# Kernel tuning notes

Hardware: AMD Instinct MI355X
Metric: run time of the kernel (lower is better)

## Reference

```python
import jax, jax.numpy as jnp
import numpy as np

B, E, NH = 32, 4096, 32
D = E // NH            # head_dim = 128
MAX_TOKENS = 2048
MAX_POS = 1536         # next_pos values in [0, MAX_POS); max pinned so max_k is static


def setup_inputs() -> dict:
    key = jax.random.key(0)
    k0, k1, k2, k3, k4, k5 = jax.random.split(key, 6)
    x = jax.random.normal(k0, (B, 1, E), jnp.float32)
    next_pos = jax.random.randint(k1, (B,), 0, MAX_POS, jnp.int32)
    next_pos = next_pos.at[0].set(MAX_POS - 1)  # pin max so sliced cache length is fixed
    scale = 0.02
    Wq = jax.random.normal(k2, (D, E), jnp.float32) * scale
    Wk = jax.random.normal(k3, (D, E), jnp.float32) * scale
    Wv = jax.random.normal(k4, (D, E), jnp.float32) * scale
    kv_cache = jax.random.normal(k5, (2, B, MAX_TOKENS, D), jnp.float32) * scale
    return {"x": x, "Wq": Wq, "Wk": Wk, "Wv": Wv, "kv_cache": kv_cache, "next_pos": next_pos}


def reference(x, Wq, Wk, Wv, kv_cache, next_pos):
    # x: (B, 1, E); torch Linear(y = x @ W.T)
    q = jnp.einsum('bse,de->bsd', x, Wq)  # (B,1,D)
    k = jnp.einsum('bse,de->bsd', x, Wk)
    v = jnp.einsum('bse,de->bsd', x, Wv)

    # scatter the new step into the cache at each sequence's next_pos
    bidx = jnp.arange(x.shape[0])
    kv = kv_cache.at[0, bidx, next_pos].set(k[:, 0])
    kv = kv.at[1, bidx, next_pos].set(v[:, 0])

    next_pos_new = next_pos + 1
    max_k = int(jax.device_get(jnp.max(next_pos_new)))  # static given pinned next_pos

    k_cache = kv[0, :, :max_k]  # (B, max_k, D)
    v_cache = kv[1, :, :max_k]

    scores = jnp.einsum('bsd,btd->bst', q, k_cache) * (D ** -0.5)  # (B,1,max_k)
    # Faithful to torch: (max_k,max_k) tril mask broadcasts scores to (B,max_k,max_k)
    tril = jnp.tril(jnp.ones((max_k, max_k), dtype=bool))
    masked = jnp.where(tril[None], scores, -jnp.inf)  # (B, max_k, max_k)
    attn = jax.nn.softmax(masked, axis=-1)
    out = attn @ v_cache  # (B, max_k, D)
    return out
```

## Files before the change

kernel.cpp:

```cpp
#include <hip/hip_runtime.h>
#include <math.h>

#define CHUNK 32

__global__ void proj_kernel(const float* __restrict__ x,
                            const float* __restrict__ Wq,
                            const float* __restrict__ Wk,
                            const float* __restrict__ Wv,
                            float* __restrict__ qkv,
                            int B, int E, int D)
{
    int d = blockIdx.x;
    int b = blockIdx.y;
    int lane = threadIdx.x;
    const float* xrow = x + (size_t)b * E;
    size_t woff = (size_t)d * E;
    float aq = 0.f, ak = 0.f, av = 0.f;
    for (int i = lane * 4; i < E; i += 64 * 4) {
        float4 x4 = *(const float4*)(xrow + i);
        float4 q4 = *(const float4*)(Wq + woff + i);
        float4 k4 = *(const float4*)(Wk + woff + i);
        float4 v4 = *(const float4*)(Wv + woff + i);
        aq += x4.x*q4.x + x4.y*q4.y + x4.z*q4.z + x4.w*q4.w;
        ak += x4.x*k4.x + x4.y*k4.y + x4.z*k4.z + x4.w*k4.w;
        av += x4.x*v4.x + x4.y*v4.y + x4.z*v4.z + x4.w*v4.w;
    }
    #pragma unroll
    for (int off = 32; off >= 1; off >>= 1) {
        aq += __shfl_xor(aq, off, 64);
        ak += __shfl_xor(ak, off, 64);
        av += __shfl_xor(av, off, 64);
    }
    if (lane == 0) {
        qkv[(size_t)b * D + d] = aq;
        qkv[((size_t)B + b) * D + d] = ak;
        qkv[((size_t)2 * B + b) * D + d] = av;
    }
}

__global__ void score_chunk_kernel(const float* __restrict__ kv,
                                   const float* __restrict__ qkv,
                                   const int* __restrict__ next_pos,
                                   float* __restrict__ s_out,
                                   float* __restrict__ m_out,
                                   float* __restrict__ l_out,
                                   float* __restrict__ acc_out,
                                   int B, int D, int T, int MT, int NC, float scale)
{
    int c = blockIdx.x;
    int b = blockIdx.y;
    int tid = threadIdx.x;
    int wave = tid >> 6;
    int lane = tid & 63;
    int l16 = lane & 15;
    int g16 = lane >> 4;

    __shared__ float s_sh[CHUNK];
    __shared__ float w_sh[CHUNK];
    __shared__ float part[2][128];

    int np = next_pos[b];
    int t0 = c * CHUNK;
    const float* q    = qkv + (size_t)b * D;
    const float* knew = qkv + ((size_t)B + b) * D;
    const float* vnew = qkv + ((size_t)2 * B + b) * D;
    const float* kbase = kv + (size_t)b * MT * D;
    const float* vbase = kv + ((size_t)B + b) * MT * D;

    float4 qa = *(const float4*)(q + l16 * 8);
    float4 qb = *(const float4*)(q + l16 * 8 + 4);

    #pragma unroll
    for (int p = 0; p < 2; ++p) {
        int j = wave * 8 + p * 4 + g16;
        int t = t0 + j;
        const float* krow = (t == np) ? knew : (kbase + (size_t)t * D);
        float4 ka = *(const float4*)(krow + l16 * 8);
        float4 kb = *(const float4*)(krow + l16 * 8 + 4);
        float ps = qa.x*ka.x + qa.y*ka.y + qa.z*ka.z + qa.w*ka.w
                 + qb.x*kb.x + qb.y*kb.y + qb.z*kb.z + qb.w*kb.w;
        ps += __shfl_xor(ps, 1, 64);
        ps += __shfl_xor(ps, 2, 64);
        ps += __shfl_xor(ps, 4, 64);
        ps += __shfl_xor(ps, 8, 64);
        if (l16 == 0) {
            float sv = (t < T) ? ps * scale : -1e30f;
            s_sh[j] = sv;
            if (t < T) s_out[(size_t)b * T + t] = sv;
        }
    }
    __syncthreads();

    if (wave == 0) {
        float sv = s_sh[lane & 31];
        float m = sv;
        #pragma unroll
        for (int off = 16; off >= 1; off >>= 1)
            m = fmaxf(m, __shfl_xor(m, off, 64));
        float w = __expf(sv - m);
        w_sh[lane & 31] = w;
        float l = w;
        #pragma unroll
        for (int off = 16; off >= 1; off >>= 1)
            l += __shfl_xor(l, off, 64);
        if (lane == 0) {
            m_out[(size_t)b * NC + c] = m;
            l_out[(size_t)b * NC + c] = l;
        }
    }
    __syncthreads();

    int gg = tid >> 7;
    int d = tid & 127;
    float a = 0.f;
    #pragma unroll
    for (int jj = 0; jj < 16; ++jj) {
        int j = gg * 16 + jj;
        int t = t0 + j;
        const float* vrow = (t == np) ? vnew : (vbase + (size_t)t * D);
        a += w_sh[j] * vrow[d];
    }
    part[gg][d] = a;
    __syncthreads();
    if (tid < 128)
        acc_out[((size_t)b * NC + c) * D + tid] = part[0][tid] + part[1][tid];
}

__global__ void out_kernel(const float* __restrict__ kv,
                           const float* __restrict__ qkv,
                           const int* __restrict__ next_pos,
                           const float* __restrict__ s_in,
                           const float* __restrict__ m_in,
                           const float* __restrict__ l_in,
                           const float* __restrict__ acc_in,
                           float* __restrict__ out,
                           int B, int D, int T, int MT, int NC)
{
    int c = blockIdx.x;
    int b = blockIdx.y;
    int tid = threadIdx.x;

    __shared__ float vs[CHUNK * 128];
    __shared__ float w_sh[CHUNK];
    __shared__ float rl_sh[CHUNK];
    __shared__ float M_sh;

    int np = next_pos[b];
    int t0 = c * CHUNK;
    const float* mrow = m_in + (size_t)b * NC;
    const float* lrow = l_in + (size_t)b * NC;

    if (tid < 64) {
        float mv = (tid <= c) ? mrow[tid] : -1e30f;
        #pragma unroll
        for (int off = 32; off >= 1; off >>= 1)
            mv = fmaxf(mv, __shfl_xor(mv, off, 64));
        if (tid == 0) M_sh = mv;
    }
    __syncthreads();
    float M = M_sh;

    const float* vbase = kv + ((size_t)B + b) * MT * D;
    const float4* vnew4 = (const float4*)(qkv + ((size_t)2 * B + b) * D);
    const float4* vbase4 = (const float4*)vbase;

    float A = 0.f;
    if (tid < 128) {
        const float* arow0 = acc_in + (size_t)b * NC * D;
        for (int cc = 0; cc < c; ++cc) {
            float e = __expf(mrow[cc] - M);
            A += e * arow0[(size_t)cc * D + tid];
        }
    } else {
        int t2 = tid - 128;
        #pragma unroll
        for (int r = 0; r < 8; ++r) {
            int i4 = t2 + r * 128;
            int j = i4 >> 5;
            int t = t0 + j;
            float4 vv = (t == np) ? vnew4[i4 & 31]
                                  : vbase4[(size_t)t * 32 + (i4 & 31)];
            ((float4*)vs)[i4] = vv;
        }
        if (t2 < CHUNK) {
            int t = t0 + t2;
            w_sh[t2] = (t < T) ? __expf(s_in[(size_t)b * T + t] - M) : 0.f;
        }
    }
    __syncthreads();

    if (tid < CHUNK) {
        float L = 0.f;
        for (int cc = 0; cc < c; ++cc)
            L += lrow[cc] * __expf(mrow[cc] - M);
        for (int r = 0; r <= tid; ++r)
            L += w_sh[r];
        rl_sh[tid] = 1.0f / L;
    }
    __syncthreads();

    if (tid < 128) {
        float* orow = out + ((size_t)b * T + t0) * (size_t)D + tid;
        #pragma unroll
        for (int j = 0; j < CHUNK; ++j) {
            int t = t0 + j;
            if (t >= T) break;
            A += w_sh[j] * vs[j * 128 + tid];
            orow[(size_t)j * D] = A * rl_sh[j];
        }
    }
}

extern "C" void kernel_launch(void* const* d_in, const int* in_sizes, int n_in,
                              void* d_out, int out_size, void* d_ws, size_t ws_size,
                              hipStream_t stream) {
    const float* x        = (const float*)d_in[0];
    const float* Wq       = (const float*)d_in[1];
    const float* Wk       = (const float*)d_in[2];
    const float* Wv       = (const float*)d_in[3];
    const float* kv       = (const float*)d_in[4];
    const int*   next_pos = (const int*)d_in[5];
    float* out = (float*)d_out;

    const int B  = in_sizes[5];
    const int E  = in_sizes[0] / B;
    const int D  = in_sizes[1] / E;
    const int T  = out_size / (B * D);
    const int MT = in_sizes[4] / (2 * B * D);
    const int NC = (T + CHUNK - 1) / CHUNK;

    float* ws   = (float*)d_ws;
    float* qkv  = ws;
    float* s    = qkv + (size_t)3 * B * D;
    float* m    = s + (size_t)B * T;
    float* l    = m + (size_t)B * NC;
    float* acc  = l + (size_t)B * NC;

    const float scale = 1.0f / sqrtf((float)D);

    proj_kernel<<<dim3(D, B), 64, 0, stream>>>(x, Wq, Wk, Wv, qkv, B, E, D);
    score_chunk_kernel<<<dim3(NC, B), 256, 0, stream>>>(kv, qkv, next_pos,
                                                        s, m, l, acc,
                                                        B, D, T, MT, NC, scale);
    out_kernel<<<dim3(NC, B), 256, 0, stream>>>(kv, qkv, next_pos,
                                                s, m, l, acc, out,
                                                B, D, T, MT, NC);
}
```

Baseline: 138.4 us.

## Add per-batch prefix scan kernel to replace quadratic carry recomputation in out_kernel

Adds a scan kernel that computes the running max, carry denominator and carry accumulator per chunk once per batch, so each out_kernel block reads its carry directly instead of looping over all previous chunks. The old approach cost work quadratic in the number of chunks. The score kernel's V accumulation is also changed to use float4 loads across 8 row groups. The cost is one extra kernel launch, a serial loop over 48 chunks in only 32 blocks, and extra workspace.

```diff
diff --git a/kernel.cpp b/kernel.cpp
--- a/kernel.cpp
+++ b/kernel.cpp
@@ -2,6 +2,7 @@
 #include <math.h>
 
 #define CHUNK 32
+#define MAXNC 128
 
 __global__ void proj_kernel(const float* __restrict__ x,
                             const float* __restrict__ Wq,
@@ -57,15 +58,15 @@
 
     __shared__ float s_sh[CHUNK];
     __shared__ float w_sh[CHUNK];
-    __shared__ float part[2][128];
+    __shared__ float part[8][128];
 
     int np = next_pos[b];
     int t0 = c * CHUNK;
     const float* q    = qkv + (size_t)b * D;
     const float* knew = qkv + ((size_t)B + b) * D;
-    const float* vnew = qkv + ((size_t)2 * B + b) * D;
     const float* kbase = kv + (size_t)b * MT * D;
-    const float* vbase = kv + ((size_t)B + b) * MT * D;
+    const float4* vnew4 = (const float4*)(qkv + ((size_t)2 * B + b) * D);
+    const float4* vbase4 = (const float4*)(kv + ((size_t)B + b) * MT * D);
 
     float4 qa = *(const float4*)(q + l16 * 8);
     float4 qb = *(const float4*)(q + l16 * 8 + 4);
@@ -110,29 +111,79 @@
     }
     __syncthreads();
 
-    int gg = tid >> 7;
-    int d = tid & 127;
-    float a = 0.f;
+    int rg = tid >> 5;
+    int d4 = tid & 31;
+    float4 a4 = make_float4(0.f, 0.f, 0.f, 0.f);
     #pragma unroll
-    for (int jj = 0; jj < 16; ++jj) {
-        int j = gg * 16 + jj;
+    for (int p = 0; p < 4; ++p) {
+        int j = rg * 4 + p;
         int t = t0 + j;
-        const float* vrow = (t == np) ? vnew : (vbase + (size_t)t * D);
-        a += w_sh[j] * vrow[d];
-    }
-    part[gg][d] = a;
-    __syncthreads();
-    if (tid < 128)
-        acc_out[((size_t)b * NC + c) * D + tid] = part[0][tid] + part[1][tid];
+        float4 vv = (t == np) ? vnew4[d4] : vbase4[(size_t)t * 32 + d4];
+        float w = w_sh[j];
+        a4.x += w * vv.x; a4.y += w * vv.y; a4.z += w * vv.z; a4.w += w * vv.w;
+    }
+    ((float4*)&part[rg][d4 * 4])[0] = a4;
+    __syncthreads();
+    if (tid < 128) {
+        float s = 0.f;
+        #pragma unroll
+        for (int r = 0; r < 8; ++r) s += part[r][tid];
+        acc_out[((size_t)b * NC + c) * D + tid] = s;
+    }
+}
+
+__global__ void scan_kernel(const float* __restrict__ m_in,
+                            const float* __restrict__ l_in,
+                            const float* __restrict__ acc_in,
+                            float* __restrict__ Mc_out,
+                            float* __restrict__ carryL_out,
+                            float* __restrict__ carryA_out,
+                            int B, int D, int NC)
+{
+    int b = blockIdx.x;
+    int tid = threadIdx.x;
+
+    extern __shared__ float sh[];
+    float* accs = sh;
+    float* m_l  = sh + (size_t)NC * 128;
+    float* l_l  = m_l + NC;
+
+    const float4* asrc = (const float4*)(acc_in + (size_t)b * NC * D);
+    float4* adst = (float4*)accs;
+    for (int i = tid; i < NC * 32; i += 128)
+        adst[i] = asrc[i];
+    if (tid < NC) {
+        m_l[tid] = m_in[(size_t)b * NC + tid];
+        l_l[tid] = l_in[(size_t)b * NC + tid];
+    }
+    __syncthreads();
+
+    float M = -1e30f, A = 0.f, L = 0.f;
+    float* caout = carryA_out + (size_t)b * NC * D + tid;
+    for (int c = 0; c < NC; ++c) {
+        float mc = m_l[c];
+        float Mn = fmaxf(M, mc);
+        float e_old = __expf(M - Mn);
+        float Ac = A * e_old;
+        caout[(size_t)c * D] = Ac;
+        if (tid == 0) {
+            Mc_out[(size_t)b * NC + c] = Mn;
+            carryL_out[(size_t)b * NC + c] = L * e_old;
+        }
+        float e_c = __expf(mc - Mn);
+        A = Ac + e_c * accs[c * 128 + tid];
+        L = L * e_old + e_c * l_l[c];
+        M = Mn;
+    }
 }
 
 __global__ void out_kernel(const float* __restrict__ kv,
                            const float* __restrict__ qkv,
                            const int* __restrict__ next_pos,
                            const float* __restrict__ s_in,
-                           const float* __restrict__ m_in,
-                           const float* __restrict__ l_in,
-                           const float* __restrict__ acc_in,
+                           const float* __restrict__ Mc_in,
+                           const float* __restrict__ carryL_in,
+                           const float* __restrict__ carryA_in,
                            float* __restrict__ out,
                            int B, int D, int T, int MT, int NC)
 {
@@ -143,33 +194,20 @@
     __shared__ float vs[CHUNK * 128];
     __shared__ float w_sh[CHUNK];
     __shared__ float rl_sh[CHUNK];
-    __shared__ float M_sh;
 
     int np = next_pos[b];
     int t0 = c * CHUNK;
-    const float* mrow = m_in + (size_t)b * NC;
-    const float* lrow = l_in + (size_t)b * NC;
-
-    if (tid < 64) {
-        float mv = (tid <= c) ? mrow[tid] : -1e30f;
-        #pragma unroll
-        for (int off = 32; off >= 1; off >>= 1)
-            mv = fmaxf(mv, __shfl_xor(mv, off, 64));
-        if (tid == 0) M_sh = mv;
-    }
-    __syncthreads();
-    float M = M_sh;
-
-    const float* vbase = kv + ((size_t)B + b) * MT * D;
+    float M = Mc_in[(size_t)b * NC + c];
+
     const float4* vnew4 = (const float4*)(qkv + ((size_t)2 * B + b) * D);
-    const float4* vbase4 = (const float4*)vbase;
+    const float4* vbase4 = (const float4*)(kv + ((size_t)B + b) * MT * D);
 
     float A = 0.f;
     if (tid < 128) {
-        const float* arow0 = acc_in + (size_t)b * NC * D;
-        for (int cc = 0; cc < c; ++cc) {
-            float e = __expf(mrow[cc] - M);
-            A += e * arow0[(size_t)cc * D + tid];
+        A = carryA_in[((size_t)b * NC + c) * D + tid];
+        if (tid < CHUNK) {
+            int t = t0 + tid;
+            w_sh[tid] = (t < T) ? __expf(s_in[(size_t)b * T + t] - M) : 0.f;
         }
     } else {
         int t2 = tid - 128;
@@ -182,17 +220,11 @@
                                   : vbase4[(size_t)t * 32 + (i4 & 31)];
             ((float4*)vs)[i4] = vv;
         }
-        if (t2 < CHUNK) {
-            int t = t0 + t2;
-            w_sh[t2] = (t < T) ? __expf(s_in[(size_t)b * T + t] - M) : 0.f;
-        }
     }
     __syncthreads();
 
     if (tid < CHUNK) {
-        float L = 0.f;
-        for (int cc = 0; cc < c; ++cc)
-            L += lrow[cc] * __expf(mrow[cc] - M);
+        float L = carryL_in[(size_t)b * NC + c];
         for (int r = 0; r <= tid; ++r)
             L += w_sh[r];
         rl_sh[tid] = 1.0f / L;
@@ -229,12 +261,15 @@
     const int MT = in_sizes[4] / (2 * B * D);
     const int NC = (T + CHUNK - 1) / CHUNK;
 
-    float* ws   = (float*)d_ws;
-    float* qkv  = ws;
-    float* s    = qkv + (size_t)3 * B * D;
-    float* m    = s + (size_t)B * T;
-    float* l    = m + (size_t)B * NC;
-    float* acc  = l + (size_t)B * NC;
+    float* ws     = (float*)d_ws;
+    float* qkv    = ws;
+    float* s      = qkv + (size_t)3 * B * D;
+    float* m      = s + (size_t)B * T;
+    float* l      = m + (size_t)B * NC;
+    float* acc    = l + (size_t)B * NC;
+    float* Mc     = acc + (size_t)B * NC * D;
+    float* carryL = Mc + (size_t)B * NC;
+    float* carryA = carryL + (size_t)B * NC;
 
     const float scale = 1.0f / sqrtf((float)D);
 
@@ -242,7 +277,10 @@
     score_chunk_kernel<<<dim3(NC, B), 256, 0, stream>>>(kv, qkv, next_pos,
                                                         s, m, l, acc,
                                                         B, D, T, MT, NC, scale);
+    size_t scan_lds = ((size_t)NC * 128 + 2 * NC) * sizeof(float);
+    scan_kernel<<<dim3(B), 128, scan_lds, stream>>>(m, l, acc, Mc, carryL, carryA,
+                                                    B, D, NC);
     out_kernel<<<dim3(NC, B), 256, 0, stream>>>(kv, qkv, next_pos,
-                                                s, m, l, acc, out,
+                                                s, Mc, carryL, carryA, out,
                                                 B, D, T, MT, NC);
 }
```

Result: faster. 135.2 us (-2.3%).

## Fuse score and output kernels with flag-based chunk prefix sync

Applied to the files above, without the earlier changes.

Merges the score-chunk and output kernels into one kernel. Each chunk block publishes its unnormalized partial V accumulator and weight sum, then spin-waits on per-chunk flags for earlier chunks of the same batch row before doing the prefix combine. The max-subtraction in the softmax is dropped and raw exp(score) is used, which relies on scores being small. The projection kernel is reorganized so each block stages one row of each weight in shared memory and reuses it across all batch rows. The risks are overflow for large scores, and deadlock if dependent blocks are not co-resident; since blocks are ordered with lower chunks first, progress is likely.

```diff
diff --git a/kernel.cpp b/kernel.cpp
--- a/kernel.cpp
+++ b/kernel.cpp
@@ -2,200 +2,219 @@
 #include <math.h>
 
 #define CHUNK 32
+
+__device__ __forceinline__ float agent_load_f(const float* p) {
+    return __hip_atomic_load(p, __ATOMIC_RELAXED, __HIP_MEMORY_SCOPE_AGENT);
+}
+__device__ __forceinline__ void agent_store_f(float* p, float v) {
+    __hip_atomic_store(p, v, __ATOMIC_RELAXED, __HIP_MEMORY_SCOPE_AGENT);
+}
 
 __global__ void proj_kernel(const float* __restrict__ x,
                             const float* __restrict__ Wq,
                             const float* __restrict__ Wk,
                             const float* __restrict__ Wv,
                             float* __restrict__ qkv,
+                            int* __restrict__ flags, int nflags,
                             int B, int E, int D)
 {
     int d = blockIdx.x;
-    int b = blockIdx.y;
-    int lane = threadIdx.x;
-    const float* xrow = x + (size_t)b * E;
-    size_t woff = (size_t)d * E;
-    float aq = 0.f, ak = 0.f, av = 0.f;
-    for (int i = lane * 4; i < E; i += 64 * 4) {
-        float4 x4 = *(const float4*)(xrow + i);
-        float4 q4 = *(const float4*)(Wq + woff + i);
-        float4 k4 = *(const float4*)(Wk + woff + i);
-        float4 v4 = *(const float4*)(Wv + woff + i);
-        aq += x4.x*q4.x + x4.y*q4.y + x4.z*q4.z + x4.w*q4.w;
-        ak += x4.x*k4.x + x4.y*k4.y + x4.z*k4.z + x4.w*k4.w;
-        av += x4.x*v4.x + x4.y*v4.y + x4.z*v4.z + x4.w*v4.w;
-    }
-    #pragma unroll
-    for (int off = 32; off >= 1; off >>= 1) {
-        aq += __shfl_xor(aq, off, 64);
-        ak += __shfl_xor(ak, off, 64);
-        av += __shfl_xor(av, off, 64);
-    }
-    if (lane == 0) {
-        qkv[(size_t)b * D + d] = aq;
-        qkv[((size_t)B + b) * D + d] = ak;
-        qkv[((size_t)2 * B + b) * D + d] = av;
-    }
-}
-
-__global__ void score_chunk_kernel(const float* __restrict__ kv,
-                                   const float* __restrict__ qkv,
-                                   const int* __restrict__ next_pos,
-                                   float* __restrict__ s_out,
-                                   float* __restrict__ m_out,
-                                   float* __restrict__ l_out,
-                                   float* __restrict__ acc_out,
-                                   int B, int D, int T, int MT, int NC, float scale)
-{
-    int c = blockIdx.x;
-    int b = blockIdx.y;
     int tid = threadIdx.x;
     int wave = tid >> 6;
     int lane = tid & 63;
-    int l16 = lane & 15;
-    int g16 = lane >> 4;
-
-    __shared__ float s_sh[CHUNK];
+    extern __shared__ float wsh[];
+
+    if (d == 0) {
+        for (int i = tid; i < nflags; i += blockDim.x) flags[i] = 0;
+    }
+
+    const float4* srcq = (const float4*)(Wq + (size_t)d * E);
+    const float4* srck = (const float4*)(Wk + (size_t)d * E);
+    const float4* srcv = (const float4*)(Wv + (size_t)d * E);
+    float4* w4 = (float4*)wsh;
+    int E4 = E >> 2;
+    for (int i = tid; i < E4; i += blockDim.x) {
+        w4[i]          = srcq[i];
+        w4[E4 + i]     = srck[i];
+        w4[2*E4 + i]   = srcv[i];
+    }
+    __syncthreads();
+
+    int b0 = wave * 4;
+    const float4* x0 = (const float4*)(x + (size_t)(b0 + 0) * E);
+    const float4* x1 = (const float4*)(x + (size_t)(b0 + 1) * E);
+    const float4* x2 = (const float4*)(x + (size_t)(b0 + 2) * E);
+    const float4* x3 = (const float4*)(x + (size_t)(b0 + 3) * E);
+
+    float aq[4] = {0,0,0,0}, ak[4] = {0,0,0,0}, av[4] = {0,0,0,0};
+    int iters = E4 >> 6;
+    for (int ii = 0; ii < iters; ++ii) {
+        int i4 = ii * 64 + lane;
+        float4 qv = w4[i4];
+        float4 kv_ = w4[E4 + i4];
+        float4 vv = w4[2*E4 + i4];
+        float4 xa = x0[i4], xb = x1[i4], xc = x2[i4], xd = x3[i4];
+        aq[0] += xa.x*qv.x + xa.y*qv.y + xa.z*qv.z + xa.w*qv.w;
+        ak[0] += xa.x*kv_.x + xa.y*kv_.y + xa.z*kv_.z + xa.w*kv_.w;
+        av[0] += xa.x*vv.x + xa.y*vv.y + xa.z*vv.z + xa.w*vv.w;
+        aq[1] += xb.x*qv.x + xb.y*qv.y + xb.z*qv.z + xb.w*qv.w;
+        ak[1] += xb.x*kv_.x + xb.y*kv_.y + xb.z*kv_.z + xb.w*kv_.w;
+        av[1] += xb.x*vv.x + xb.y*vv.y + xb.z*vv.z + xb.w*vv.w;
+        aq[2] += xc.x*qv.x + xc.y*qv.y + xc.z*qv.z + xc.w*qv.w;
+        ak[2] += xc.x*kv_.x + xc.y*kv_.y + xc.z*kv_.z + xc.w*kv_.w;
+        av[2] += xc.x*vv.x + xc.y*vv.y + xc.z*vv.z + xc.w*vv.w;
+        aq[3] += xd.x*qv.x + xd.y*qv.y + xd.z*qv.z + xd.w*qv.w;
+        ak[3] += xd.x*kv_.x + xd.y*kv_.y + xd.z*kv_.z + xd.w*kv_.w;
+        av[3] += xd.x*vv.x + xd.y*vv.y + xd.z*vv.z + xd.w*vv.w;
+    }
+    #pragma unroll
+    for (int u = 0; u < 4; ++u) {
+        #pragma unroll
+        for (int off = 32; off >= 1; off >>= 1) {
+            aq[u] += __shfl_xor(aq[u], off, 64);
+            ak[u] += __shfl_xor(ak[u], off, 64);
+            av[u] += __shfl_xor(av[u], off, 64);
+        }
+    }
+    if (lane == 0) {
+        #pragma unroll
+        for (int u = 0; u < 4; ++u) {
+            int b = b0 + u;
+            qkv[(size_t)b * D + d]            = aq[u];
+            qkv[((size_t)B + b) * D + d]      = ak[u];
+            qkv[((size_t)2 * B + b) * D + d]  = av[u];
+        }
+    }
+}
+
+__global__ void __launch_bounds__(256)
+fused_attn_kernel(const float* __restrict__ kv,
+                  const float* __restrict__ qkv,
+                  const int* __restrict__ next_pos,
+                  float* __restrict__ accpub,
+                  float* __restrict__ lpub,
+                  int* __restrict__ flags,
+                  float* __restrict__ out,
+                  int B, int D, int T, int MT, int NC, float scale)
+{
+    int bid = blockIdx.x;
+    int b = bid / NC;
+    int c = bid - b * NC;
+    int tid = threadIdx.x;
+    int wave = tid >> 6, lane = tid & 63;
+    int l16 = lane & 15, g16 = lane >> 4;
+
+    __shared__ float vs[CHUNK * 128];
     __shared__ float w_sh[CHUNK];
-    __shared__ float part[2][128];
+    __shared__ float rl_sh[CHUNK];
+    __shared__ float Lc_sh;
 
     int np = next_pos[b];
     int t0 = c * CHUNK;
-    const float* q    = qkv + (size_t)b * D;
-    const float* knew = qkv + ((size_t)B + b) * D;
-    const float* vnew = qkv + ((size_t)2 * B + b) * D;
+    const float* q     = qkv + (size_t)b * D;
+    const float* knew  = qkv + ((size_t)B + b) * D;
     const float* kbase = kv + (size_t)b * MT * D;
-    const float* vbase = kv + ((size_t)B + b) * MT * D;
+    const float4* vnew4  = (const float4*)(qkv + ((size_t)2 * B + b) * D);
+    const float4* vbase4 = (const float4*)(kv + ((size_t)B + b) * MT * D);
 
     float4 qa = *(const float4*)(q + l16 * 8);
     float4 qb = *(const float4*)(q + l16 * 8 + 4);
 
-    #pragma unroll
-    for (int p = 0; p < 2; ++p) {
-        int j = wave * 8 + p * 4 + g16;
-        int t = t0 + j;
-        const float* krow = (t == np) ? knew : (kbase + (size_t)t * D);
-        float4 ka = *(const float4*)(krow + l16 * 8);
-        float4 kb = *(const float4*)(krow + l16 * 8 + 4);
-        float ps = qa.x*ka.x + qa.y*ka.y + qa.z*ka.z + qa.w*ka.w
-                 + qb.x*kb.x + qb.y*kb.y + qb.z*kb.z + qb.w*kb.w;
+    int j0 = wave * 8 + g16, j1 = j0 + 4;
+    int ta = t0 + j0, tb = t0 + j1;
+    const float* kra = (ta == np) ? knew : (kbase + (size_t)ta * D);
+    const float* krb = (tb == np) ? knew : (kbase + (size_t)tb * D);
+    float4 ka0 = *(const float4*)(kra + l16 * 8);
+    float4 kb0 = *(const float4*)(kra + l16 * 8 + 4);
+    float4 ka1 = *(const float4*)(krb + l16 * 8);
+    float4 kb1 = *(const float4*)(krb + l16 * 8 + 4);
+
+    float4 sv0, sv1, sv2, sv3;
+    {
+        int i4, t;
+        i4 = tid;       t = t0 + (i4 >> 5);
+        sv0 = (t == np) ? vnew4[i4 & 31] : vbase4[(size_t)t * 32 + (i4 & 31)];
+        i4 = tid + 256; t = t0 + (i4 >> 5);
+        sv1 = (t == np) ? vnew4[i4 & 31] : vbase4[(size_t)t * 32 + (i4 & 31)];
+        i4 = tid + 512; t = t0 + (i4 >> 5);
+        sv2 = (t == np) ? vnew4[i4 & 31] : vbase4[(size_t)t * 32 + (i4 & 31)];
+        i4 = tid + 768; t = t0 + (i4 >> 5);
+        sv3 = (t == np) ? vnew4[i4 & 31] : vbase4[(size_t)t * 32 + (i4 & 31)];
+    }
+
+    {
+        float ps = qa.x*ka0.x + qa.y*ka0.y + qa.z*ka0.z + qa.w*ka0.w
+                 + qb.x*kb0.x + qb.y*kb0.y + qb.z*kb0.z + qb.w*kb0.w;
         ps += __shfl_xor(ps, 1, 64);
         ps += __shfl_xor(ps, 2, 64);
         ps += __shfl_xor(ps, 4, 64);
         ps += __shfl_xor(ps, 8, 64);
-        if (l16 == 0) {
-            float sv = (t < T) ? ps * scale : -1e30f;
-            s_sh[j] = sv;
-            if (t < T) s_out[(size_t)b * T + t] = sv;
-        }
-    }
-    __syncthreads();
-
-    if (wave == 0) {
-        float sv = s_sh[lane & 31];
-        float m = sv;
-        #pragma unroll
-        for (int off = 16; off >= 1; off >>= 1)
-            m = fmaxf(m, __shfl_xor(m, off, 64));
-        float w = __expf(sv - m);
-        w_sh[lane & 31] = w;
-        float l = w;
-        #pragma unroll
-        for (int off = 16; off >= 1; off >>= 1)
-            l += __shfl_xor(l, off, 64);
-        if (lane == 0) {
-            m_out[(size_t)b * NC + c] = m;
-            l_out[(size_t)b * NC + c] = l;
-        }
-    }
-    __syncthreads();
-
-    int gg = tid >> 7;
-    int d = tid & 127;
-    float a = 0.f;
-    #pragma unroll
-    for (int jj = 0; jj < 16; ++jj) {
-        int j = gg * 16 + jj;
-        int t = t0 + j;
-        const float* vrow = (t == np) ? vnew : (vbase + (size_t)t * D);
-        a += w_sh[j] * vrow[d];
-    }
-    part[gg][d] = a;
-    __syncthreads();
-    if (tid < 128)
-        acc_out[((size_t)b * NC + c) * D + tid] = part[0][tid] + part[1][tid];
-}
-
-__global__ void out_kernel(const float* __restrict__ kv,
-                           const float* __restrict__ qkv,
-                           const int* __restrict__ next_pos,
-                           const float* __restrict__ s_in,
-                           const float* __restrict__ m_in,
-                           const float* __restrict__ l_in,
-                           const float* __restrict__ acc_in,
-                           float* __restrict__ out,
-                           int B, int D, int T, int MT, int NC)
-{
-    int c = blockIdx.x;
-    int b = blockIdx.y;
-    int tid = threadIdx.x;
-
-    __shared__ float vs[CHUNK * 128];
-    __shared__ float w_sh[CHUNK];
-    __shared__ float rl_sh[CHUNK];
-    __shared__ float M_sh;
-
-    int np = next_pos[b];
-    int t0 = c * CHUNK;
-    const float* mrow = m_in + (size_t)b * NC;
-    const float* lrow = l_in + (size_t)b * NC;
-
-    if (tid < 64) {
-        float mv = (tid <= c) ? mrow[tid] : -1e30f;
+        if (l16 == 0) w_sh[j0] = __expf(ps * scale);
+
+        float pt = qa.x*ka1.x + qa.y*ka1.y + qa.z*ka1.z + qa.w*ka1.w
+                 + qb.x*kb1.x + qb.y*kb1.y + qb.z*kb1.z + qb.w*kb1.w;
+        pt += __shfl_xor(pt, 1, 64);
+        pt += __shfl_xor(pt, 2, 64);
+        pt += __shfl_xor(pt, 4, 64);
+        pt += __shfl_xor(pt, 8, 64);
+        if (l16 == 0) w_sh[j1] = __expf(pt * scale);
+    }
+    ((float4*)vs)[tid]       = sv0;
+    ((float4*)vs)[tid + 256] = sv1;
+    ((float4*)vs)[tid + 512] = sv2;
+    ((float4*)vs)[tid + 768] = sv3;
+    __syncthreads();
+
+    if (tid < 128) {
+        float a = 0.f;
+        #pragma unroll
+        for (int j = 0; j < CHUNK; ++j)
+            a += w_sh[j] * vs[j * 128 + tid];
+        agent_store_f(accpub + (size_t)bid * 128 + tid, a);
+    } else if (tid < 192) {
+        int j = tid - 128;
+        float lw = (j < CHUNK) ? w_sh[j] : 0.f;
         #pragma unroll
         for (int off = 32; off >= 1; off >>= 1)
-            mv = fmaxf(mv, __shfl_xor(mv, off, 64));
-        if (tid == 0) M_sh = mv;
-    }
-    __syncthreads();
-    float M = M_sh;
-
-    const float* vbase = kv + ((size_t)B + b) * MT * D;
-    const float4* vnew4 = (const float4*)(qkv + ((size_t)2 * B + b) * D);
-    const float4* vbase4 = (const float4*)vbase;
+            lw += __shfl_xor(lw, off, 64);
+        if (j == 0) agent_store_f(lpub + bid, lw);
+    }
+    __syncthreads();
+    if (tid == 0)
+        __hip_atomic_store(flags + bid, 1, __ATOMIC_RELEASE, __HIP_MEMORY_SCOPE_AGENT);
+
+    if (tid < 64 && tid < c) {
+        const int* fp = flags + b * NC + tid;
+        while (__hip_atomic_load(fp, __ATOMIC_RELAXED, __HIP_MEMORY_SCOPE_AGENT) == 0)
+            __builtin_amdgcn_s_sleep(2);
+    }
+    __syncthreads();
 
     float A = 0.f;
     if (tid < 128) {
-        const float* arow0 = acc_in + (size_t)b * NC * D;
-        for (int cc = 0; cc < c; ++cc) {
-            float e = __expf(mrow[cc] - M);
-            A += e * arow0[(size_t)cc * D + tid];
-        }
-    } else {
-        int t2 = tid - 128;
-        #pragma unroll
-        for (int r = 0; r < 8; ++r) {
-            int i4 = t2 + r * 128;
-            int j = i4 >> 5;
-            int t = t0 + j;
-            float4 vv = (t == np) ? vnew4[i4 & 31]
-                                  : vbase4[(size_t)t * 32 + (i4 & 31)];
-            ((float4*)vs)[i4] = vv;
-        }
-        if (t2 < CHUNK) {
-            int t = t0 + t2;
-            w_sh[t2] = (t < T) ? __expf(s_in[(size_t)b * T + t] - M) : 0.f;
-        }
+        const float* ap = accpub + (size_t)(b * NC) * 128 + tid;
+        #pragma unroll 8
+        for (int cc = 0; cc < c; ++cc)
+            A += agent_load_f(ap + (size_t)cc * 128);
+    } else if (tid < 192) {
+        int cc = tid - 128;
+        float lv = (cc < c) ? agent_load_f(lpub + b * NC + cc) : 0.f;
+        #pragma unroll
+        for (int off = 32; off >= 1; off >>= 1)
+            lv += __shfl_xor(lv, off, 64);
+        if (cc == 0) Lc_sh = lv;
     }
     __syncthreads();
 
     if (tid < CHUNK) {
-        float L = 0.f;
-        for (int cc = 0; cc < c; ++cc)
-            L += lrow[cc] * __expf(mrow[cc] - M);
-        for (int r = 0; r <= tid; ++r)
-            L += w_sh[r];
-        rl_sh[tid] = 1.0f / L;
+        float wv = w_sh[tid];
+        float xacc = wv;
+        #pragma unroll
+        for (int off = 1; off < 32; off <<= 1) {
+            float n = __shfl_up(xacc, off, 64);
+            if (tid >= off) xacc += n;
+        }
+        rl_sh[tid] = 1.0f / (Lc_sh + xacc);
     }
     __syncthreads();
 
@@ -203,8 +222,6 @@
         float* orow = out + ((size_t)b * T + t0) * (size_t)D + tid;
         #pragma unroll
         for (int j = 0; j < CHUNK; ++j) {
-            int t = t0 + j;
-            if (t >= T) break;
             A += w_sh[j] * vs[j * 128 + tid];
             orow[(size_t)j * D] = A * rl_sh[j];
         }
@@ -227,22 +244,19 @@
     const int D  = in_sizes[1] / E;
     const int T  = out_size / (B * D);
     const int MT = in_sizes[4] / (2 * B * D);
-    const int NC = (T + CHUNK - 1) / CHUNK;
-
-    float* ws   = (float*)d_ws;
-    float* qkv  = ws;
-    float* s    = qkv + (size_t)3 * B * D;
-    float* m    = s + (size_t)B * T;
-    float* l    = m + (size_t)B * NC;
-    float* acc  = l + (size_t)B * NC;
+    const int NC = T / CHUNK;
+
+    float* ws     = (float*)d_ws;
+    float* qkv    = ws;
+    float* accpub = qkv + (size_t)3 * B * D;
+    float* lpub   = accpub + (size_t)B * NC * D;
+    int*   flags  = (int*)(lpub + (size_t)B * NC);
 
     const float scale = 1.0f / sqrtf((float)D);
 
-    proj_kernel<<<dim3(D, B), 64, 0, stream>>>(x, Wq, Wk, Wv, qkv, B, E, D);
-    score_chunk_kernel<<<dim3(NC, B), 256, 0, stream>>>(kv, qkv, next_pos,
-                                                        s, m, l, acc,
-                                                        B, D, T, MT, NC, scale);
-    out_kernel<<<dim3(NC, B), 256, 0, stream>>>(kv, qkv, next_pos,
-                                                s, m, l, acc, out,
-                                                B, D, T, MT, NC);
-}
+    proj_kernel<<<dim3(D), 512, (size_t)3 * E * sizeof(float), stream>>>(
+        x, Wq, Wk, Wv, qkv, flags, B * NC, B, E, D);
+    fused_attn_kernel<<<dim3(B * NC), 256, 0, stream>>>(
+        kv, qkv, next_pos, accpub, lpub, flags, out,
+        B, D, T, MT, NC, scale);
+}
```

Result: slower. 183.1 us (+32.3%).
